# Optimization experiments

Measured on AMD Instinct MI355X. Metric: run time of the kernel, lower is better.

The kernel has to match this reference:

```python
import jax, jax.numpy as jnp
import numpy as np

B, H_HIST, S_DIM, HID, G, K, A = 1024, 16384, 32, 64, 10, 4, 8


def setup_inputs() -> dict:
    key = jax.random.key(0)
    ks = jax.random.split(key, 12)
    inp = {
        'state_batch': jax.random.normal(ks[0], (B, S_DIM), jnp.float32),
        'state_history_batch': jax.random.normal(ks[1], (H_HIST, S_DIM), jnp.float32),
        'joint_action_history_batch': jax.random.normal(ks[2], (H_HIST, G, A), jnp.float32),
        # per-abstract-agent encoder MLP: Linear(S->H) + ReLU, Linear(H->H) + ReLU, Linear(H->H) + ReLU
        'W0': jax.random.normal(ks[3], (K, S_DIM, HID), jnp.float32) / np.sqrt(S_DIM),
        'b0': jax.random.normal(ks[4], (K, HID), jnp.float32) * 0.01,
        'W1': jax.random.normal(ks[5], (K, HID, HID), jnp.float32) / np.sqrt(HID),
        'b1': jax.random.normal(ks[6], (K, HID), jnp.float32) * 0.01,
        'W2': jax.random.normal(ks[7], (K, HID, HID), jnp.float32) / np.sqrt(HID),
        'b2': jax.random.normal(ks[8], (K, HID), jnp.float32) * 0.01,
        'assignment_matrix': jnp.ones((G, K), jnp.float32),
    }
    return inp


def _encode(x, W0, b0, W1, b1, W2, b2):
    # x: [N, S_DIM] shared across K encoders -> [K, N, HID]
    h = jax.nn.relu(jnp.einsum('ni,kio->kno', x, W0) + b0[:, None, :])
    h = jax.nn.relu(jnp.einsum('kni,kio->kno', h, W1) + b1[:, None, :])
    h = jax.nn.relu(jnp.einsum('kni,kio->kno', h, W2) + b2[:, None, :])
    return h


def reference(state_batch, state_history_batch, joint_action_history_batch,
              W0, b0, W1, b1, W2, b2, assignment_matrix):
    enc_s = _encode(state_batch, W0, b0, W1, b1, W2, b2)            # [K, B, HID]
    enc_h = _encode(state_history_batch, W0, b0, W1, b1, W2, b2)    # [K, H, HID]
    # per (abstract agent k, batch item b): softmax over history of <enc_h, enc_s>
    attn = jax.nn.softmax(jnp.einsum('khd,kbd->kbh', enc_h, enc_s), axis=-1)  # [K, B, H]
    # weighted action aggregation: [H,G,A] contracted over H
    abs_pred = jnp.einsum('kbh,hga->kbga', attn, joint_action_history_batch)  # [K, B, G, A]
    soft_assign = jax.nn.softmax(assignment_matrix, axis=-1)                  # [G, K]
    out = jnp.einsum('gk,kbga->bga', soft_assign, abs_pred)                   # [B, G, A]
    return out
```

## Files before the change

kernel.cpp:

```cpp
#include <hip/hip_runtime.h>
#include <stdint.h>

#define B_SZ 1024
#define H_SZ 16384
#define SD   32
#define HID  64
#define G_SZ 10
#define K_SZ 4
#define A_SZ 8
#define VA   80
#define NC   16

typedef float f32x4  __attribute__((ext_vector_type(4)));
typedef short bf16x8 __attribute__((ext_vector_type(8)));

__device__ inline short f2bf(float a) {
    unsigned u = __float_as_uint(a);
    return (short)((u + 0x7FFFu + ((u >> 16) & 1u)) >> 16);
}
__device__ inline void split_bf(float v, short& hi, short& lo) {
    hi = f2bf(v);
    lo = f2bf(v - __uint_as_float(((unsigned)(unsigned short)hi) << 16));
}
__device__ inline int cvt_pk_bf16(float a, float b) {
    int r;
    asm("v_cvt_pk_bf16_f32 %0, %1, %2" : "=v"(r) : "v"(a), "v"(b));
    return r;
}
__device__ inline void split2(float f0, float f1, int& hi, int& lo) {
    hi = cvt_pk_bf16(f0, f1);
    float r0 = f0 - __uint_as_float((unsigned)hi << 16);
    float r1 = f1 - __uint_as_float((unsigned)hi & 0xFFFF0000u);
    lo = cvt_pk_bf16(r0, r1);
}

__global__ __launch_bounds__(256) void k_prep(
    const float* __restrict__ W0, const float* __restrict__ W1,
    const float* __restrict__ W2,
    short* __restrict__ w0h, short* __restrict__ w0l,
    short* __restrict__ w1h, short* __restrict__ w1l,
    short* __restrict__ w2h, short* __restrict__ w2l)
{
    int idx = blockIdx.x * 256 + threadIdx.x;
    short hh, ll;
    if (idx < 8192) {
        int k = idx >> 11, r = idx & 2047;
        int i = r >> 6, jj = r & 63;
        int tt = jj >> 4, l15 = jj & 15;
        int quad = (i >> 3) & 3, e = i & 7;
        split_bf(W0[k * 2048 + i * 64 + jj], hh, ll);
        int dst = k * 2048 + tt * 512 + (quad * 16 + l15) * 8 + e;
        w0h[dst] = hh; w0l[dst] = ll;
    } else if (idx < 24576) {
        int d = idx - 8192;
        int k = d >> 12, r = d & 4095;
        int i = r >> 6, jj = r & 63;
        int kb = i >> 5, quad = (i >> 3) & 3, e = i & 7;
        int tt = jj >> 4, l15 = jj & 15;
        split_bf(W1[k * 4096 + i * 64 + jj], hh, ll);
        int dst = k * 4096 + tt * 1024 + kb * 512 + (quad * 16 + l15) * 8 + e;
        w1h[dst] = hh; w1l[dst] = ll;
    } else if (idx < 40960) {
        int d = idx - 24576;
        int k = d >> 12, r = d & 4095;
        int i = r >> 6, jj = r & 63;
        int kb = i >> 5, quad = (i >> 3) & 3, e = i & 7;
        int tt = jj >> 4, l15 = jj & 15;
        split_bf(W2[k * 4096 + i * 64 + jj], hh, ll);
        int dst = k * 4096 + tt * 1024 + kb * 512 + (quad * 16 + l15) * 8 + e;
        w2h[dst] = hh; w2l[dst] = ll;
    }
}

__global__ __launch_bounds__(256, 3) void k_encode(
    const float* __restrict__ state, const float* __restrict__ hist,
    const float* __restrict__ act,
    const short* __restrict__ w0fh, const short* __restrict__ w0fl,
    const short* __restrict__ w1fh, const short* __restrict__ w1fl,
    const short* __restrict__ w2fh, const short* __restrict__ w2fl,
    const float* __restrict__ b0, const float* __restrict__ b1,
    const float* __restrict__ b2,
    short* __restrict__ enc_s_h, short* __restrict__ enc_s_l,
    short* __restrict__ kf_h, short* __restrict__ kf_l,
    short* __restrict__ vf_h, short* __restrict__ vf_l)
{
    __shared__ __align__(16) short smem[18432];
    const int bid = blockIdx.x;
    const int t = threadIdx.x;

    if (bid >= 1088) {
        short* tile_h = smem;
        short* tile_l = smem + 5376;
        const int h0 = (bid - 1088) * 64;
        #pragma unroll
        for (int i = 0; i < 10; ++i) {
            int idx2 = 2 * (t + i * 256);
            float2 v = *(const float2*)(act + (size_t)h0 * VA + idx2);
            int h = idx2 / 80, c = idx2 - h * 80;
            int hi, lo; split2(v.x, v.y, hi, lo);
            *(int*)(tile_h + h * 84 + c) = hi;
            *(int*)(tile_l + h * 84 + c) = lo;
        }
        __syncthreads();
        #pragma unroll
        for (int i = 0; i < 3; ++i) {
            int jj = t + i * 256;
            if (jj < 640) {
                int va = jj >> 3, hb = jj & 7;
                union { short s[8]; uint4 v; } uh, ul;
                #pragma unroll
                for (int uu = 0; uu < 8; ++uu) {
                    uh.s[uu] = tile_h[(hb * 8 + uu) * 84 + va];
                    ul.s[uu] = tile_l[(hb * 8 + uu) * 84 + va];
                }
                int vtile = (h0 >> 5) + (hb >> 2);
                int lanep = ((hb & 3) << 4) | (va & 15);
                size_t a = (size_t)vtile * 2560 + (va >> 4) * 512 + lanep * 8;
                *(uint4*)(vf_h + a) = uh.v;
                *(uint4*)(vf_l + a) = ul.v;
            }
        }
        return;
    }

    const int k = bid / 272;
    const int tl = bid % 272;
    const bool is_state = (tl < 16);
    const float qscale = is_state ? 1.44269504f : 1.0f;
    const float* X = is_state ? state + (size_t)tl * 64 * SD
                              : hist + (size_t)(tl - 16) * 64 * SD;
    short* dst_h = enc_s_h + ((size_t)k * B_SZ + tl * 64) * HID;
    short* dst_l = enc_s_l + ((size_t)k * B_SZ + tl * 64) * HID;

    short* xt_h  = smem;
    short* xt_l  = smem + 2560;
    short* hb2_h = smem;
    short* hb2_l = smem + 4608;
    short* hb1_h = smem + 9216;
    short* hb1_l = smem + 13824;
    short* ot_h  = smem + 9216;
    short* ot_l  = smem + 13824;

    {
        int r = t >> 2, c0 = (t & 3) * 8;
        const float* src = X + r * SD + c0;
        #pragma unroll
        for (int u = 0; u < 4; ++u) {
            float2 v = *(const float2*)(src + 2 * u);
            int hi, lo; split2(v.x, v.y, hi, lo);
            *(int*)(xt_h + r * 40 + c0 + 2 * u) = hi;
            *(int*)(xt_l + r * 40 + c0 + 2 * u) = lo;
        }
    }
    __syncthreads();

    const int w = t >> 6, l15 = t & 15, quad = (t >> 4) & 3, lane = t & 63;
    const f32x4 fz = {0.f, 0.f, 0.f, 0.f};
    const int row0 = w * 16 + quad * 4;

    {
        bf16x8 xa_h = *(const bf16x8*)(xt_h + (w * 16 + l15) * 40 + quad * 8);
        bf16x8 xa_l = *(const bf16x8*)(xt_l + (w * 16 + l15) * 40 + quad * 8);
        const float* b0k = b0 + k * HID;
        const short* wbh = w0fh + k * 2048 + lane * 8;
        const short* wbl = w0fl + k * 2048 + lane * 8;
        #pragma unroll
        for (int tt = 0; tt < 4; ++tt) {
            bf16x8 wf_h = *(const bf16x8*)(wbh + tt * 512);
            bf16x8 wf_l = *(const bf16x8*)(wbl + tt * 512);
            f32x4 c = __builtin_amdgcn_mfma_f32_16x16x32_bf16(xa_h, wf_h, fz, 0, 0, 0);
            c = __builtin_amdgcn_mfma_f32_16x16x32_bf16(xa_l, wf_h, c, 0, 0, 0);
            c = __builtin_amdgcn_mfma_f32_16x16x32_bf16(xa_h, wf_l, c, 0, 0, 0);
            float bias = b0k[l15 + 16 * tt];
            float f0 = fmaxf(c[0] + bias, 0.f), f1 = fmaxf(c[1] + bias, 0.f);
            float f2 = fmaxf(c[2] + bias, 0.f), f3 = fmaxf(c[3] + bias, 0.f);
            int h01, l01, h23, l23;
            split2(f0, f1, h01, l01); split2(f2, f3, h23, l23);
            int cc = l15 + 16 * tt;
            hb1_h[(row0    ) * 72 + cc] = (short)h01;
            hb1_h[(row0 + 1) * 72 + cc] = (short)(h01 >> 16);
            hb1_h[(row0 + 2) * 72 + cc] = (short)h23;
            hb1_h[(row0 + 3) * 72 + cc] = (short)(h23 >> 16);
            hb1_l[(row0    ) * 72 + cc] = (short)l01;
            hb1_l[(row0 + 1) * 72 + cc] = (short)(l01 >> 16);
            hb1_l[(row0 + 2) * 72 + cc] = (short)l23;
            hb1_l[(row0 + 3) * 72 + cc] = (short)(l23 >> 16);
        }
    }
    __syncthreads();
    {
        bf16x8 ha0_h = *(const bf16x8*)(hb1_h + (w * 16 + l15) * 72 + quad * 8);
        bf16x8 ha0_l = *(const bf16x8*)(hb1_l + (w * 16 + l15) * 72 + quad * 8);
        bf16x8 ha1_h = *(const bf16x8*)(hb1_h + (w * 16 + l15) * 72 + 32 + quad * 8);
        bf16x8 ha1_l = *(const bf16x8*)(hb1_l + (w * 16 + l15) * 72 + 32 + quad * 8);
        const float* b1k = b1 + k * HID;
        const short* wbh = w1fh + k * 4096 + lane * 8;
        const short* wbl = w1fl + k * 4096 + lane * 8;
        #pragma unroll
        for (int tt = 0; tt < 4; ++tt) {
            bf16x8 wfa_h = *(const bf16x8*)(wbh + tt * 1024);
            bf16x8 wfb_h = *(const bf16x8*)(wbh + tt * 1024 + 512);
            bf16x8 wfa_l = *(const bf16x8*)(wbl + tt * 1024);
            bf16x8 wfb_l = *(const bf16x8*)(wbl + tt * 1024 + 512);
            f32x4 c = __builtin_amdgcn_mfma_f32_16x16x32_bf16(ha0_h, wfa_h, fz, 0, 0, 0);
            c = __builtin_amdgcn_mfma_f32_16x16x32_bf16(ha1_h, wfb_h, c, 0, 0, 0);
            c = __builtin_amdgcn_mfma_f32_16x16x32_bf16(ha0_l, wfa_h, c, 0, 0, 0);
            c = __builtin_amdgcn_mfma_f32_16x16x32_bf16(ha1_l, wfb_h, c, 0, 0, 0);
            c = __builtin_amdgcn_mfma_f32_16x16x32_bf16(ha0_h, wfa_l, c, 0, 0, 0);
            c = __builtin_amdgcn_mfma_f32_16x16x32_bf16(ha1_h, wfb_l, c, 0, 0, 0);
            float bias = b1k[l15 + 16 * tt];
            float f0 = fmaxf(c[0] + bias, 0.f), f1 = fmaxf(c[1] + bias, 0.f);
            float f2 = fmaxf(c[2] + bias, 0.f), f3 = fmaxf(c[3] + bias, 0.f);
            int h01, l01, h23, l23;
            split2(f0, f1, h01, l01); split2(f2, f3, h23, l23);
            int cc = l15 + 16 * tt;
            hb2_h[(row0    ) * 72 + cc] = (short)h01;
            hb2_h[(row0 + 1) * 72 + cc] = (short)(h01 >> 16);
            hb2_h[(row0 + 2) * 72 + cc] = (short)h23;
            hb2_h[(row0 + 3) * 72 + cc] = (short)(h23 >> 16);
            hb2_l[(row0    ) * 72 + cc] = (short)l01;
            hb2_l[(row0 + 1) * 72 + cc] = (short)(l01 >> 16);
            hb2_l[(row0 + 2) * 72 + cc] = (short)l23;
            hb2_l[(row0 + 3) * 72 + cc] = (short)(l23 >> 16);
        }
    }
    __syncthreads();
    {
        bf16x8 ha0_h = *(const bf16x8*)(hb2_h + (w * 16 + l15) * 72 + quad * 8);
        bf16x8 ha0_l = *(const bf16x8*)(hb2_l + (w * 16 + l15) * 72 + quad * 8);
        bf16x8 ha1_h = *(const bf16x8*)(hb2_h + (w * 16 + l15) * 72 + 32 + quad * 8);
        bf16x8 ha1_l = *(const bf16x8*)(hb2_l + (w * 16 + l15) * 72 + 32 + quad * 8);
        const float* b2k = b2 + k * HID;
        const short* wbh = w2fh + k * 4096 + lane * 8;
        const short* wbl = w2fl + k * 4096 + lane * 8;
        #pragma unroll
        for (int tt = 0; tt < 4; ++tt) {
            bf16x8 wfa_h = *(const bf16x8*)(wbh + tt * 1024);
            bf16x8 wfb_h = *(const bf16x8*)(wbh + tt * 1024 + 512);
            bf16x8 wfa_l = *(const bf16x8*)(wbl + tt * 1024);
            bf16x8 wfb_l = *(const bf16x8*)(wbl + tt * 1024 + 512);
            f32x4 c = __builtin_amdgcn_mfma_f32_16x16x32_bf16(ha0_h, wfa_h, fz, 0, 0, 0);
            c = __builtin_amdgcn_mfma_f32_16x16x32_bf16(ha1_h, wfb_h, c, 0, 0, 0);
            c = __builtin_amdgcn_mfma_f32_16x16x32_bf16(ha0_l, wfa_h, c, 0, 0, 0);
            c = __builtin_amdgcn_mfma_f32_16x16x32_bf16(ha1_l, wfb_h, c, 0, 0, 0);
            c = __builtin_amdgcn_mfma_f32_16x16x32_bf16(ha0_h, wfa_l, c, 0, 0, 0);
            c = __builtin_amdgcn_mfma_f32_16x16x32_bf16(ha1_h, wfb_l, c, 0, 0, 0);
            float bias = b2k[l15 + 16 * tt];
            float f0 = fmaxf(c[0] + bias, 0.f) * qscale;
            float f1 = fmaxf(c[1] + bias, 0.f) * qscale;
            float f2 = fmaxf(c[2] + bias, 0.f) * qscale;
            float f3 = fmaxf(c[3] + bias, 0.f) * qscale;
            int h01, l01, h23, l23;
            split2(f0, f1, h01, l01); split2(f2, f3, h23, l23);
            int cc = l15 + 16 * tt;
            ot_h[(row0    ) * 72 + cc] = (short)h01;
            ot_h[(row0 + 1) * 72 + cc] = (short)(h01 >> 16);
            ot_h[(row0 + 2) * 72 + cc] = (short)h23;
            ot_h[(row0 + 3) * 72 + cc] = (short)(h23 >> 16);
            ot_l[(row0    ) * 72 + cc] = (short)l01;
            ot_l[(row0 + 1) * 72 + cc] = (short)(l01 >> 16);
            ot_l[(row0 + 2) * 72 + cc] = (short)l23;
            ot_l[(row0 + 3) * 72 + cc] = (short)(l23 >> 16);
        }
    }
    __syncthreads();
    if (is_state) {
        #pragma unroll
        for (int u = 0; u < 2; ++u) {
            int id = t * 2 + u;
            int row = id >> 3, c0 = (id & 7) * 8;
            *(uint4*)(dst_h + row * HID + c0) = *(const uint4*)(ot_h + row * 72 + c0);
            *(uint4*)(dst_l + row * HID + c0) = *(const uint4*)(ot_l + row * 72 + c0);
        }
    } else {
        const int ktbase = k * 512 + (tl - 16) * 2;
        #pragma unroll
        for (int u = 0; u < 2; ++u) {
            int id = t * 2 + u;
            int kt2 = id >> 8;
            int f2 = (id >> 6) & 3;
            int lanep = id & 63;
            int hl = kt2 * 32 + ((f2 >> 1) & 1) * 16 + (lanep & 15);
            int c0 = (f2 & 1) * 32 + ((lanep >> 4) & 3) * 8;
            size_t a = (size_t)(ktbase + kt2) * 2048 + f2 * 512 + (size_t)lanep * 8;
            *(uint4*)(kf_h + a) = *(const uint4*)(ot_h + hl * 72 + c0);
            *(uint4*)(kf_l + a) = *(const uint4*)(ot_l + hl * 72 + c0);
        }
    }
}

template<int NCt>
__global__ __launch_bounds__(256, 2) void k_flash(
    const short* __restrict__ enc_s_h, const short* __restrict__ enc_s_l,
    const short* __restrict__ kf_h, const short* __restrict__ kf_l,
    const short* __restrict__ vf_h, const short* __restrict__ vf_l,
    float* __restrict__ Pm, float* __restrict__ Pl, float* __restrict__ Pacc)
{
    constexpr int CHt = H_SZ / NCt;
    constexpr int NT = CHt / 32;
    static_assert(NT % 2 == 0, "NT must be even for 2x unroll");

    const int bid = blockIdx.x;
    const int r8 = bid & 7, j = bid >> 3;
    const int mtile = j & 7, grp = j >> 3;
    const int idx = grp * 8 + r8;
    const int k = idx / NCt, chunk = idx % NCt;
    const int t = threadIdx.x, w = t >> 6, lane = t & 63;
    const int l15 = t & 15, quad = (t >> 4) & 3;
    const int q0 = mtile * 128 + w * 32;
    const f32x4 fz = {0.f, 0.f, 0.f, 0.f};

    bf16x8 qh[2][2], ql[2][2];
    #pragma unroll
    for (int sub = 0; sub < 2; ++sub)
        #pragma unroll
        for (int kb = 0; kb < 2; ++kb) {
            size_t off = ((size_t)k * B_SZ + q0 + sub * 16 + l15) * HID + kb * 32 + quad * 8;
            qh[sub][kb] = *(const bf16x8*)(enc_s_h + off);
            ql[sub][kb] = *(const bf16x8*)(enc_s_l + off);
        }

    f32x4 acc[2][5];
    #pragma unroll
    for (int s = 0; s < 2; ++s)
        #pragma unroll
        for (int tt = 0; tt < 5; ++tt) acc[s][tt] = fz;
    float mrun[2] = {-__builtin_inff(), -__builtin_inff()};
    float lrun[2] = {0.f, 0.f};

    const int tile0 = chunk * NT;
    const short* kbh = kf_h + ((size_t)(k * 512 + tile0)) * 2048 + lane * 8;
    const short* kbl = kf_l + ((size_t)(k * 512 + tile0)) * 2048 + lane * 8;
    const short* vbh = vf_h + (size_t)tile0 * 2560 + lane * 8;
    const short* vbl = vf_l + (size_t)tile0 * 2560 + lane * 8;

    bf16x8 kA[8], kB[8];
    #pragma unroll
    for (int f = 0; f < 4; ++f) {
        kA[f]     = *(const bf16x8*)(kbh + f * 512);
        kA[4 + f] = *(const bf16x8*)(kbl + f * 512);
    }

    auto body = [&](bf16x8 (&kc)[8], bf16x8 (&kn)[8], int it) {
        bf16x8 vh[5], vl[5];
        const short* vph = vbh + (size_t)it * 2560;
        const short* vpl = vbl + (size_t)it * 2560;
        #pragma unroll
        for (int tt = 0; tt < 3; ++tt) {
            vh[tt] = *(const bf16x8*)(vph + tt * 512);
            vl[tt] = *(const bf16x8*)(vpl + tt * 512);
        }
        if (it + 1 < NT) {
            const short* nph = kbh + (size_t)(it + 1) * 2048;
            const short* npl = kbl + (size_t)(it + 1) * 2048;
            #pragma unroll
            for (int f = 0; f < 4; ++f) {
                kn[f]     = *(const bf16x8*)(nph + f * 512);
                kn[4 + f] = *(const bf16x8*)(npl + f * 512);
            }
        }

        f32x4 S[2][2];
        __builtin_amdgcn_s_setprio(1);
        #pragma unroll
        for (int sub = 0; sub < 2; ++sub) {
            f32x4 c = __builtin_amdgcn_mfma_f32_16x16x32_bf16(kc[0], qh[sub][0], fz, 0, 0, 0);
            c = __builtin_amdgcn_mfma_f32_16x16x32_bf16(kc[1], qh[sub][1], c, 0, 0, 0);
            c = __builtin_amdgcn_mfma_f32_16x16x32_bf16(kc[4], qh[sub][0], c, 0, 0, 0);
            c = __builtin_amdgcn_mfma_f32_16x16x32_bf16(kc[5], qh[sub][1], c, 0, 0, 0);
            c = __builtin_amdgcn_mfma_f32_16x16x32_bf16(kc[0], ql[sub][0], c, 0, 0, 0);
            c = __builtin_amdgcn_mfma_f32_16x16x32_bf16(kc[1], ql[sub][1], c, 0, 0, 0);
            S[sub][0] = c;
            f32x4 d = __builtin_amdgcn_mfma_f32_16x16x32_bf16(kc[2], qh[sub][0], fz, 0, 0, 0);
            d = __builtin_amdgcn_mfma_f32_16x16x32_bf16(kc[3], qh[sub][1], d, 0, 0, 0);
            d = __builtin_amdgcn_mfma_f32_16x16x32_bf16(kc[6], qh[sub][0], d, 0, 0, 0);
            d = __builtin_amdgcn_mfma_f32_16x16x32_bf16(kc[7], qh[sub][1], d, 0, 0, 0);
            d = __builtin_amdgcn_mfma_f32_16x16x32_bf16(kc[2], ql[sub][0], d, 0, 0, 0);
            d = __builtin_amdgcn_mfma_f32_16x16x32_bf16(kc[3], ql[sub][1], d, 0, 0, 0);
            S[sub][1] = d;
        }
        __builtin_amdgcn_s_setprio(0);

        #pragma unroll
        for (int tt = 3; tt < 5; ++tt) {
            vh[tt] = *(const bf16x8*)(vph + tt * 512);
            vl[tt] = *(const bf16x8*)(vpl + tt * 512);
        }

        bf16x8 pfv[2];
        #pragma unroll
        for (int sub = 0; sub < 2; ++sub) {
            f32x4 slo = S[sub][0], shi = S[sub][1];
            float a3 = fmaxf(fmaxf(slo[0], slo[1]), slo[2]);
            float b3 = fmaxf(fmaxf(slo[3], shi[0]), shi[1]);
            float c3 = fmaxf(fmaxf(shi[2], shi[3]), a3);
            float tm = fmaxf(b3, c3);
            tm = fmaxf(tm, __shfl_xor(tm, 16));
            tm = fmaxf(tm, __shfl_xor(tm, 32));
            if (__any(tm > mrun[sub])) {
                float mnew = fmaxf(mrun[sub], tm);
                float alpha = exp2f(mrun[sub] - mnew);
                lrun[sub] *= alpha;
                #pragma unroll
                for (int tt = 0; tt < 5; ++tt) acc[sub][tt] = acc[sub][tt] * alpha;
                mrun[sub] = mnew;
            }
            float m = mrun[sub];
            float p0 = exp2f(slo[0] - m), p1 = exp2f(slo[1] - m);
            float p2 = exp2f(slo[2] - m), p3 = exp2f(slo[3] - m);
            float p4 = exp2f(shi[0] - m), p5 = exp2f(shi[1] - m);
            float p6 = exp2f(shi[2] - m), p7 = exp2f(shi[3] - m);
            float ps = (p0 + p1) + (p2 + p3) + (p4 + p5) + (p6 + p7);
            ps += __shfl_xor(ps, 16);
            ps += __shfl_xor(ps, 32);
            lrun[sub] += ps;

            int plo01 = cvt_pk_bf16(p0, p1), plo23 = cvt_pk_bf16(p2, p3);
            int phi01 = cvt_pk_bf16(p4, p5), phi23 = cvt_pk_bf16(p6, p7);
            union { int i[4]; bf16x8 v; } pf;
            #pragma unroll
            for (int jj = 0; jj < 4; ++jj) {
                int src = (((2 * quad + (jj >> 1)) & 3) << 4) + l15;
                int glo = __shfl((jj & 1) ? plo23 : plo01, src);
                int ghi = __shfl((jj & 1) ? phi23 : phi01, src);
                pf.i[jj] = (quad >= 2) ? ghi : glo;
            }
            pfv[sub] = pf.v;
        }

        __builtin_amdgcn_s_setprio(1);
        #pragma unroll
        for (int tt = 0; tt < 5; ++tt) {
            acc[0][tt] = __builtin_amdgcn_mfma_f32_16x16x32_bf16(vh[tt], pfv[0], acc[0][tt], 0, 0, 0);
            acc[0][tt] = __builtin_amdgcn_mfma_f32_16x16x32_bf16(vl[tt], pfv[0], acc[0][tt], 0, 0, 0);
            acc[1][tt] = __builtin_amdgcn_mfma_f32_16x16x32_bf16(vh[tt], pfv[1], acc[1][tt], 0, 0, 0);
            acc[1][tt] = __builtin_amdgcn_mfma_f32_16x16x32_bf16(vl[tt], pfv[1], acc[1][tt], 0, 0, 0);
        }
        __builtin_amdgcn_s_setprio(0);
    };

    for (int ii = 0; ii < NT; ii += 2) {
        body(kA, kB, ii);
        body(kB, kA, ii + 1);
    }

    const int qg = k * B_SZ + q0;
    #pragma unroll
    for (int sub = 0; sub < 2; ++sub) {
        int q = qg + sub * 16 + l15;
        if (quad == 0) {
            Pm[chunk * 4096 + q] = mrun[sub];
            Pl[chunk * 4096 + q] = lrun[sub];
        }
        #pragma unroll
        for (int tt = 0; tt < 5; ++tt)
            #pragma unroll
            for (int r = 0; r < 4; ++r) {
                int va = tt * 16 + quad * 4 + r;
                Pacc[((size_t)chunk * VA + va) * 4096 + q] = acc[sub][tt][r];
            }
    }
}

__global__ __launch_bounds__(256) void k_reduce(
    const float* __restrict__ Pm, const float* __restrict__ Pl,
    const float* __restrict__ Pacc, const float* __restrict__ assign,
    float* __restrict__ out)
{
    const int bid = blockIdx.x;
    const int qb = bid / 20, vcg = bid - qb * 20;
    const int t = threadIdx.x;
    const int b = qb * 64 + (t & 63);
    const int va = vcg * 4 + (t >> 6);
    const int g = va >> 3;

    float mc[K_SZ][NC];
    float M[K_SZ] = {-__builtin_inff(), -__builtin_inff(),
                     -__builtin_inff(), -__builtin_inff()};
    #pragma unroll
    for (int c = 0; c < NC; ++c)
        #pragma unroll
        for (int k = 0; k < K_SZ; ++k) {
            float m = Pm[c * 4096 + k * B_SZ + b];
            mc[k][c] = m;
            M[k] = fmaxf(M[k], m);
        }
    float L[K_SZ] = {0.f, 0.f, 0.f, 0.f};
    #pragma unroll
    for (int c = 0; c < NC; ++c)
        #pragma unroll
        for (int k = 0; k < K_SZ; ++k) {
            float wv = exp2f(mc[k][c] - M[k]);
            mc[k][c] = wv;
            L[k] += wv * Pl[c * 4096 + k * B_SZ + b];
        }
    float o[K_SZ] = {0.f, 0.f, 0.f, 0.f};
    #pragma unroll
    for (int c = 0; c < NC; ++c)
        #pragma unroll
        for (int k = 0; k < K_SZ; ++k)
            o[k] += mc[k][c] * Pacc[((size_t)(c * VA + va)) * 4096 + k * B_SZ + b];

    float a0 = assign[g * K_SZ + 0], a1 = assign[g * K_SZ + 1];
    float a2 = assign[g * K_SZ + 2], a3 = assign[g * K_SZ + 3];
    float mx = fmaxf(fmaxf(a0, a1), fmaxf(a2, a3));
    const float L2E = 1.44269504f;
    float e0 = exp2f((a0 - mx) * L2E), e1 = exp2f((a1 - mx) * L2E);
    float e2 = exp2f((a2 - mx) * L2E), e3 = exp2f((a3 - mx) * L2E);
    float inv = 1.f / (e0 + e1 + e2 + e3);
    float r = e0 * inv * (o[0] / L[0]) + e1 * inv * (o[1] / L[1])
            + e2 * inv * (o[2] / L[2]) + e3 * inv * (o[3] / L[3]);
    out[(size_t)b * VA + va] = r;
}

extern "C" void kernel_launch(void* const* d_in, const int* in_sizes, int n_in,
                              void* d_out, int out_size, void* d_ws, size_t ws_size,
                              hipStream_t stream)
{
    const float* state  = (const float*)d_in[0];
    const float* hist   = (const float*)d_in[1];
    const float* act    = (const float*)d_in[2];
    const float* W0     = (const float*)d_in[3];
    const float* b0     = (const float*)d_in[4];
    const float* W1     = (const float*)d_in[5];
    const float* b1     = (const float*)d_in[6];
    const float* W2     = (const float*)d_in[7];
    const float* b2     = (const float*)d_in[8];
    const float* assign = (const float*)d_in[9];
    float* out = (float*)d_out;

    char* ws = (char*)d_ws;
    short* enc_s_h = (short*)(ws);
    short* enc_s_l = (short*)(ws + 524288);
    short* kf_h    = (short*)(ws + 1048576);
    short* kf_l    = (short*)(ws + 9437184);
    short* vf_h    = (short*)(ws + 17825792);
    short* vf_l    = (short*)(ws + 20447232);
    const size_t base = 23068672;

    float* Pm   = (float*)(ws + base);
    float* Pl   = (float*)(ws + base + 262144);
    float* Pacc = (float*)(ws + base + 524288);
    char*  wt   = ws + base + 524288 + 20971520;
    short* w0fh = (short*)(wt);
    short* w0fl = (short*)(wt + 16384);
    short* w1fh = (short*)(wt + 32768);
    short* w1fl = (short*)(wt + 65536);
    short* w2fh = (short*)(wt + 98304);
    short* w2fl = (short*)(wt + 131072);

    k_prep<<<160, 256, 0, stream>>>(W0, W1, W2, w0fh, w0fl, w1fh, w1fl, w2fh, w2fl);
    k_encode<<<1344, 256, 0, stream>>>(state, hist, act,
                                       w0fh, w0fl, w1fh, w1fl, w2fh, w2fl,
                                       b0, b1, b2,
                                       enc_s_h, enc_s_l, kf_h, kf_l, vf_h, vf_l);
    k_flash<NC><<<512, 256, 0, stream>>>(enc_s_h, enc_s_l, kf_h, kf_l,
                                         vf_h, vf_l, Pm, Pl, Pacc);
    k_reduce<<<320, 256, 0, stream>>>(Pm, Pl, Pacc, assign, out);
}
```

Before: 155.1 us.

## Split flash kernel into single-wave blocks with one 16-query tile each

Restructures k_flash from 256-thread blocks (4 waves, each handling two 16-query subtiles) into 64-thread blocks that each handle a single 16-query tile, launching 4096 blocks instead of 512. This cuts per-wave register use (half the accumulators, Q fragments and softmax state) and raises the number of independent waves for latency hiding. In exchange, each K/V tile is now loaded once per 16 queries instead of once per 32, which doubles K/V fragment traffic through the caches and halves MFMA work per load.

```diff
diff --git a/kernel.cpp b/kernel.cpp
--- a/kernel.cpp
+++ b/kernel.cpp
@@ -290,7 +290,7 @@
 }
 
 template<int NCt>
-__global__ __launch_bounds__(256, 2) void k_flash(
+__global__ __launch_bounds__(64, 2) void k_flash(
     const short* __restrict__ enc_s_h, const short* __restrict__ enc_s_l,
     const short* __restrict__ kf_h, const short* __restrict__ kf_l,
     const short* __restrict__ vf_h, const short* __restrict__ vf_l,
@@ -302,37 +302,33 @@
 
     const int bid = blockIdx.x;
     const int r8 = bid & 7, j = bid >> 3;
-    const int mtile = j & 7, grp = j >> 3;
+    const int qt = j & 63, grp = j >> 6;
     const int idx = grp * 8 + r8;
     const int k = idx / NCt, chunk = idx % NCt;
-    const int t = threadIdx.x, w = t >> 6, lane = t & 63;
+    const int t = threadIdx.x;
     const int l15 = t & 15, quad = (t >> 4) & 3;
-    const int q0 = mtile * 128 + w * 32;
+    const int q0 = qt * 16;
     const f32x4 fz = {0.f, 0.f, 0.f, 0.f};
 
-    bf16x8 qh[2][2], ql[2][2];
-    #pragma unroll
-    for (int sub = 0; sub < 2; ++sub)
-        #pragma unroll
-        for (int kb = 0; kb < 2; ++kb) {
-            size_t off = ((size_t)k * B_SZ + q0 + sub * 16 + l15) * HID + kb * 32 + quad * 8;
-            qh[sub][kb] = *(const bf16x8*)(enc_s_h + off);
-            ql[sub][kb] = *(const bf16x8*)(enc_s_l + off);
-        }
-
-    f32x4 acc[2][5];
-    #pragma unroll
-    for (int s = 0; s < 2; ++s)
-        #pragma unroll
-        for (int tt = 0; tt < 5; ++tt) acc[s][tt] = fz;
-    float mrun[2] = {-__builtin_inff(), -__builtin_inff()};
-    float lrun[2] = {0.f, 0.f};
+    bf16x8 qh[2], ql[2];
+    #pragma unroll
+    for (int kb = 0; kb < 2; ++kb) {
+        size_t off = ((size_t)k * B_SZ + q0 + l15) * HID + kb * 32 + quad * 8;
+        qh[kb] = *(const bf16x8*)(enc_s_h + off);
+        ql[kb] = *(const bf16x8*)(enc_s_l + off);
+    }
+
+    f32x4 acc[5];
+    #pragma unroll
+    for (int tt = 0; tt < 5; ++tt) acc[tt] = fz;
+    float mrun = -__builtin_inff();
+    float lrun = 0.f;
 
     const int tile0 = chunk * NT;
-    const short* kbh = kf_h + ((size_t)(k * 512 + tile0)) * 2048 + lane * 8;
-    const short* kbl = kf_l + ((size_t)(k * 512 + tile0)) * 2048 + lane * 8;
-    const short* vbh = vf_h + (size_t)tile0 * 2560 + lane * 8;
-    const short* vbl = vf_l + (size_t)tile0 * 2560 + lane * 8;
+    const short* kbh = kf_h + ((size_t)(k * 512 + tile0)) * 2048 + t * 8;
+    const short* kbl = kf_l + ((size_t)(k * 512 + tile0)) * 2048 + t * 8;
+    const short* vbh = vf_h + (size_t)tile0 * 2560 + t * 8;
+    const short* vbl = vf_l + (size_t)tile0 * 2560 + t * 8;
 
     bf16x8 kA[8], kB[8];
     #pragma unroll
@@ -360,24 +356,23 @@
             }
         }
 
-        f32x4 S[2][2];
+        f32x4 slo, shi;
         __builtin_amdgcn_s_setprio(1);
-        #pragma unroll
-        for (int sub = 0; sub < 2; ++sub) {
-            f32x4 c = __builtin_amdgcn_mfma_f32_16x16x32_bf16(kc[0], qh[sub][0], fz, 0, 0, 0);
-            c = __builtin_amdgcn_mfma_f32_16x16x32_bf16(kc[1], qh[sub][1], c, 0, 0, 0);
-            c = __builtin_amdgcn_mfma_f32_16x16x32_bf16(kc[4], qh[sub][0], c, 0, 0, 0);
-            c = __builtin_amdgcn_mfma_f32_16x16x32_bf16(kc[5], qh[sub][1], c, 0, 0, 0);
-            c = __builtin_amdgcn_mfma_f32_16x16x32_bf16(kc[0], ql[sub][0], c, 0, 0, 0);
-            c = __builtin_amdgcn_mfma_f32_16x16x32_bf16(kc[1], ql[sub][1], c, 0, 0, 0);
-            S[sub][0] = c;
-            f32x4 d = __builtin_amdgcn_mfma_f32_16x16x32_bf16(kc[2], qh[sub][0], fz, 0, 0, 0);
-            d = __builtin_amdgcn_mfma_f32_16x16x32_bf16(kc[3], qh[sub][1], d, 0, 0, 0);
-            d = __builtin_amdgcn_mfma_f32_16x16x32_bf16(kc[6], qh[sub][0], d, 0, 0, 0);
-            d = __builtin_amdgcn_mfma_f32_16x16x32_bf16(kc[7], qh[sub][1], d, 0, 0, 0);
-            d = __builtin_amdgcn_mfma_f32_16x16x32_bf16(kc[2], ql[sub][0], d, 0, 0, 0);
-            d = __builtin_amdgcn_mfma_f32_16x16x32_bf16(kc[3], ql[sub][1], d, 0, 0, 0);
-            S[sub][1] = d;
+        {
+            f32x4 c = __builtin_amdgcn_mfma_f32_16x16x32_bf16(kc[0], qh[0], fz, 0, 0, 0);
+            c = __builtin_amdgcn_mfma_f32_16x16x32_bf16(kc[1], qh[1], c, 0, 0, 0);
+            c = __builtin_amdgcn_mfma_f32_16x16x32_bf16(kc[4], qh[0], c, 0, 0, 0);
+            c = __builtin_amdgcn_mfma_f32_16x16x32_bf16(kc[5], qh[1], c, 0, 0, 0);
+            c = __builtin_amdgcn_mfma_f32_16x16x32_bf16(kc[0], ql[0], c, 0, 0, 0);
+            c = __builtin_amdgcn_mfma_f32_16x16x32_bf16(kc[1], ql[1], c, 0, 0, 0);
+            slo = c;
+            f32x4 d = __builtin_amdgcn_mfma_f32_16x16x32_bf16(kc[2], qh[0], fz, 0, 0, 0);
+            d = __builtin_amdgcn_mfma_f32_16x16x32_bf16(kc[3], qh[1], d, 0, 0, 0);
+            d = __builtin_amdgcn_mfma_f32_16x16x32_bf16(kc[6], qh[0], d, 0, 0, 0);
+            d = __builtin_amdgcn_mfma_f32_16x16x32_bf16(kc[7], qh[1], d, 0, 0, 0);
+            d = __builtin_amdgcn_mfma_f32_16x16x32_bf16(kc[2], ql[0], d, 0, 0, 0);
+            d = __builtin_amdgcn_mfma_f32_16x16x32_bf16(kc[3], ql[1], d, 0, 0, 0);
+            shi = d;
         }
         __builtin_amdgcn_s_setprio(0);
 
@@ -387,25 +382,23 @@
             vl[tt] = *(const bf16x8*)(vpl + tt * 512);
         }
 
-        bf16x8 pfv[2];
-        #pragma unroll
-        for (int sub = 0; sub < 2; ++sub) {
-            f32x4 slo = S[sub][0], shi = S[sub][1];
+        bf16x8 pfv;
+        {
             float a3 = fmaxf(fmaxf(slo[0], slo[1]), slo[2]);
             float b3 = fmaxf(fmaxf(slo[3], shi[0]), shi[1]);
             float c3 = fmaxf(fmaxf(shi[2], shi[3]), a3);
             float tm = fmaxf(b3, c3);
             tm = fmaxf(tm, __shfl_xor(tm, 16));
             tm = fmaxf(tm, __shfl_xor(tm, 32));
-            if (__any(tm > mrun[sub])) {
-                float mnew = fmaxf(mrun[sub], tm);
-                float alpha = exp2f(mrun[sub] - mnew);
-                lrun[sub] *= alpha;
+            if (__any(tm > mrun)) {
+                float mnew = fmaxf(mrun, tm);
+                float alpha = exp2f(mrun - mnew);
+                lrun *= alpha;
                 #pragma unroll
-                for (int tt = 0; tt < 5; ++tt) acc[sub][tt] = acc[sub][tt] * alpha;
-                mrun[sub] = mnew;
+                for (int tt = 0; tt < 5; ++tt) acc[tt] = acc[tt] * alpha;
+                mrun = mnew;
             }
-            float m = mrun[sub];
+            float m = mrun;
             float p0 = exp2f(slo[0] - m), p1 = exp2f(slo[1] - m);
             float p2 = exp2f(slo[2] - m), p3 = exp2f(slo[3] - m);
             float p4 = exp2f(shi[0] - m), p5 = exp2f(shi[1] - m);
@@ -413,7 +406,7 @@
             float ps = (p0 + p1) + (p2 + p3) + (p4 + p5) + (p6 + p7);
             ps += __shfl_xor(ps, 16);
             ps += __shfl_xor(ps, 32);
-            lrun[sub] += ps;
+            lrun += ps;
 
             int plo01 = cvt_pk_bf16(p0, p1), plo23 = cvt_pk_bf16(p2, p3);
             int phi01 = cvt_pk_bf16(p4, p5), phi23 = cvt_pk_bf16(p6, p7);
@@ -425,16 +418,14 @@
                 int ghi = __shfl((jj & 1) ? phi23 : phi01, src);
                 pf.i[jj] = (quad >= 2) ? ghi : glo;
             }
-            pfv[sub] = pf.v;
+            pfv = pf.v;
         }
 
         __builtin_amdgcn_s_setprio(1);
         #pragma unroll
         for (int tt = 0; tt < 5; ++tt) {
-            acc[0][tt] = __builtin_amdgcn_mfma_f32_16x16x32_bf16(vh[tt], pfv[0], acc[0][tt], 0, 0, 0);
-            acc[0][tt] = __builtin_amdgcn_mfma_f32_16x16x32_bf16(vl[tt], pfv[0], acc[0][tt], 0, 0, 0);
-            acc[1][tt] = __builtin_amdgcn_mfma_f32_16x16x32_bf16(vh[tt], pfv[1], acc[1][tt], 0, 0, 0);
-            acc[1][tt] = __builtin_amdgcn_mfma_f32_16x16x32_bf16(vl[tt], pfv[1], acc[1][tt], 0, 0, 0);
+            acc[tt] = __builtin_amdgcn_mfma_f32_16x16x32_bf16(vh[tt], pfv, acc[tt], 0, 0, 0);
+            acc[tt] = __builtin_amdgcn_mfma_f32_16x16x32_bf16(vl[tt], pfv, acc[tt], 0, 0, 0);
         }
         __builtin_amdgcn_s_setprio(0);
     };
@@ -444,22 +435,18 @@
         body(kB, kA, ii + 1);
     }
 
-    const int qg = k * B_SZ + q0;
-    #pragma unroll
-    for (int sub = 0; sub < 2; ++sub) {
-        int q = qg + sub * 16 + l15;
-        if (quad == 0) {
-            Pm[chunk * 4096 + q] = mrun[sub];
-            Pl[chunk * 4096 + q] = lrun[sub];
-        }
-        #pragma unroll
-        for (int tt = 0; tt < 5; ++tt)
-            #pragma unroll
-            for (int r = 0; r < 4; ++r) {
-                int va = tt * 16 + quad * 4 + r;
-                Pacc[((size_t)chunk * VA + va) * 4096 + q] = acc[sub][tt][r];
-            }
-    }
+    const int q = k * B_SZ + q0 + l15;
+    if (quad == 0) {
+        Pm[chunk * 4096 + q] = mrun;
+        Pl[chunk * 4096 + q] = lrun;
+    }
+    #pragma unroll
+    for (int tt = 0; tt < 5; ++tt)
+        #pragma unroll
+        for (int r = 0; r < 4; ++r) {
+            int va = tt * 16 + quad * 4 + r;
+            Pacc[((size_t)chunk * VA + va) * 4096 + q] = acc[tt][r];
+        }
 }
 
 __global__ __launch_bounds__(256) void k_reduce(
@@ -554,7 +541,7 @@
                                        w0fh, w0fl, w1fh, w1fl, w2fh, w2fl,
                                        b0, b1, b2,
                                        enc_s_h, enc_s_l, kf_h, kf_l, vf_h, vf_l);
-    k_flash<NC><<<512, 256, 0, stream>>>(enc_s_h, enc_s_l, kf_h, kf_l,
+    k_flash<NC><<<4096, 64, 0, stream>>>(enc_s_h, enc_s_l, kf_h, kf_l,
                                          vf_h, vf_l, Pm, Pl, Pacc);
     k_reduce<<<320, 256, 0, stream>>>(Pm, Pl, Pacc, assign, out);
 }
```

Measured after the change: 177.7 us. 1.15x slower.
